# Kernel tuning notes

Measured on AMD Instinct MI355X. Metric: run time of the kernel, lower is better.

The kernel has to match this reference:

```python
import jax, jax.numpy as jnp
import numpy as np
from jax import lax

B, S, E = 512, 128, 7
H = 1024
PRED_LEN = 96


def setup_inputs() -> dict:
    key = jax.random.key(0)
    ks = jax.random.split(key, 10)
    u = lambda k, shape: jax.random.uniform(k, shape, jnp.float32, -0.1, 0.1)
    return {
        "x": jax.random.normal(ks[0], (B, S, E), jnp.float32),
        "Wi0": u(ks[1], (4 * H, E)),
        "Wh0": u(ks[2], (4 * H, H)),
        "b0": u(ks[3], (4 * H,)),
        "Wi1": u(ks[4], (4 * H, H)),
        "Wh1": u(ks[5], (4 * H, H)),
        "b1": u(ks[6], (4 * H,)),
        "Wfc": u(ks[7], (PRED_LEN * E, H)),
        "bfc": u(ks[8], (PRED_LEN * E,)),
    }


def _lstm_layer(xs, Wi, Wh, b):
    # xs: [B, S, in] -> hs: [B, S, H]; gate order i, f, g, o
    batch = xs.shape[0]
    hidden = Wh.shape[1]
    # precompute input projections for all timesteps in one big GEMM
    x_proj = jnp.einsum("bsi,gi->bsg", xs, Wi) + b  # [B, S, 4H]

    def step(carry, xp_t):
        h, c = carry
        gates = xp_t + h @ Wh.T  # [B, 4H]
        i_t, f_t, g_t, o_t = jnp.split(gates, 4, axis=-1)
        i_t = jax.nn.sigmoid(i_t)
        f_t = jax.nn.sigmoid(f_t)
        g_t = jnp.tanh(g_t)
        o_t = jax.nn.sigmoid(o_t)
        c = f_t * c + i_t * g_t
        h = o_t * jnp.tanh(c)
        return (h, c), h

    h0 = jnp.zeros((batch, hidden), xs.dtype)
    c0 = jnp.zeros((batch, hidden), xs.dtype)
    (_, _), hs = lax.scan(step, (h0, c0), jnp.swapaxes(x_proj, 0, 1))
    return jnp.swapaxes(hs, 0, 1)  # [B, S, H]


def reference(x, Wi0, Wh0, b0, Wi1, Wh1, b1, Wfc, bfc):
    h1 = _lstm_layer(x, Wi0, Wh0, b0)
    h2 = _lstm_layer(h1, Wi1, Wh1, b1)
    last = h2[:, -1, :]  # [B, H]
    pred = last @ Wfc.T + bfc  # [B, PRED_LEN*E]
    return pred.reshape(x.shape[0], PRED_LEN, E)
```

## Files before the change

### kernel.cpp

```cpp
#include <hip/hip_runtime.h>
#include <hip/hip_bf16.h>


typedef __bf16 bf16x8 __attribute__((ext_vector_type(8)));
typedef float  f32x4  __attribute__((ext_vector_type(4)));

#define HSZ   (512 * 1024)

__device__ __forceinline__ float sigm_f(float x) {
    x = fminf(30.f, fmaxf(-30.f, x));
    return 1.0f / (1.0f + __expf(-x));
}
__device__ __forceinline__ float tanh_f(float x) {
    x = fminf(30.f, fmaxf(-30.f, x));
    float e = __expf(-2.0f * x);
    return (1.0f - e) / (1.0f + e);
}

__device__ __forceinline__ int perm_row(int np) {
    int g = (np >> 4) & 3;
    int j = ((np >> 6) << 4) | (np & 15);
    return g * 1024 + j;
}

__device__ __forceinline__ void spin_ge(const int* p, int target) {
    while (__hip_atomic_load(p, __ATOMIC_RELAXED, __HIP_MEMORY_SCOPE_AGENT) < target)
        __builtin_amdgcn_s_sleep(1);
}
__device__ __forceinline__ void signal_inc(int* p) {
    __hip_atomic_fetch_add(p, 1, __ATOMIC_RELAXED, __HIP_MEMORY_SCOPE_AGENT);
}
__device__ __forceinline__ void inv_l1() {
    asm volatile("buffer_inv" ::: "memory");
}
__device__ __forceinline__ void store_ea(unsigned* p, unsigned v) {
    __hip_atomic_store(p, v, __ATOMIC_RELAXED, __HIP_MEMORY_SCOPE_AGENT);
}


__global__ void prep_w0(const float* __restrict__ Wh0, __bf16* __restrict__ W0p) {
    int idx = blockIdx.x * 256 + threadIdx.x;
    int np = idx >> 8, k4 = (idx & 255) << 2;
    int r = perm_row(np);
    float4 v = *(const float4*)(Wh0 + r * 1024 + k4);
    __bf16* o = W0p + np * 1024 + k4;
    o[0] = (__bf16)v.x; o[1] = (__bf16)v.y; o[2] = (__bf16)v.z; o[3] = (__bf16)v.w;
}

__global__ void prep_w1(const float* __restrict__ Wi1, const float* __restrict__ Wh1,
                        __bf16* __restrict__ W1p) {
    int idx = blockIdx.x * 256 + threadIdx.x;
    int np = idx >> 9, k4 = (idx & 511) << 2;
    int r = perm_row(np);
    const float* s = (k4 < 1024) ? (Wi1 + r * 1024 + k4) : (Wh1 + r * 1024 + (k4 - 1024));
    float4 v = *(const float4*)s;
    __bf16* o = W1p + np * 2048 + k4;
    o[0] = (__bf16)v.x; o[1] = (__bf16)v.y; o[2] = (__bf16)v.z; o[3] = (__bf16)v.w;
}

__global__ void prep_wfc(const float* __restrict__ Wfc, __bf16* __restrict__ Wfcp) {
    int idx = blockIdx.x * 256 + threadIdx.x;
    int n = idx >> 8, k4 = (idx & 255) << 2;
    __bf16* o = Wfcp + n * 1024 + k4;
    if (n < 672) {
        float4 v = *(const float4*)(Wfc + n * 1024 + k4);
        o[0] = (__bf16)v.x; o[1] = (__bf16)v.y; o[2] = (__bf16)v.z; o[3] = (__bf16)v.w;
    } else {
        o[0] = (__bf16)0.f; o[1] = (__bf16)0.f; o[2] = (__bf16)0.f; o[3] = (__bf16)0.f;
    }
}

__global__ void prep_small(const float* __restrict__ Wi0, const float* __restrict__ b0,
                           const float* __restrict__ b1,
                           float* __restrict__ Wi0p, float* __restrict__ b1p) {
    int np = blockIdx.x * 256 + threadIdx.x;
    int r = perm_row(np);
    float* o = Wi0p + np * 8;
    #pragma unroll
    for (int q = 0; q < 7; ++q) o[q] = Wi0[r * 7 + q];
    o[7] = b0[r];
    b1p[np] = b1[r];
}


template <bool D0, bool D1>
__device__ __forceinline__ void floop(const __bf16* __restrict__ abase,
                                      const __bf16* __restrict__ w0row,
                                      const __bf16* __restrict__ w1row,
                                      int tid,
                                      char* AldsB, char* B0ldsB, char* B1ldsB,
                                      f32x4 (&acc0)[4], f32x4 (&acc1)[4]) {
    const int a_r = tid >> 3;
    const int a_c = (tid & 7) << 3;
    const int b_r = tid >> 2;
    const int b_c = (tid & 3) << 4;
    const int l  = tid & 63, w = tid >> 6;
    const int wm = w & 3,   wn = w >> 2;
    const int lj = l & 15,  lq = l >> 4;
    const int r7 = lj & 7;

    const __bf16* arw = abase + a_r * 1024 + a_c;

    const int awr  = a_r * 128 + (((tid & 7) ^ (a_r & 7)) << 4);
    const int bwr0 = b_r * 128 + (((((tid & 3) << 1) | 0) ^ (b_r & 7)) << 4);
    const int bwr1 = b_r * 128 + (((((tid & 3) << 1) | 1) ^ (b_r & 7)) << 4);
    const int rc0 = ((lq     ) ^ r7) << 4;
    const int rc1 = ((lq | 4 ) ^ r7) << 4;

    uint4 ra, rb00, rb01, rb10, rb11;
    auto ld = [&](int k0) {
        ra = *(const uint4*)(arw + k0);
        if (D0) {
            const __bf16* p = w0row + k0;
            rb00 = *(const uint4*)(p);
            rb01 = *(const uint4*)(p + 8);
        }
        if (D1) {
            const __bf16* p = w1row + k0;
            rb10 = *(const uint4*)(p);
            rb11 = *(const uint4*)(p + 8);
        }
    };
    auto wr = [&](int buf) {
        *(uint4*)(AldsB + buf * 8192 + awr) = ra;
        if (D0) {
            char* Bl = B0ldsB + buf * 16384;
            *(uint4*)(Bl + bwr0) = rb00;
            *(uint4*)(Bl + bwr1) = rb01;
        }
        if (D1) {
            char* Bl = B1ldsB + buf * 16384;
            *(uint4*)(Bl + bwr0) = rb10;
            *(uint4*)(Bl + bwr1) = rb11;
        }
    };

    ld(0);
    wr(0);
    ld(64);
    __syncthreads();

    const char* Ap  = AldsB  + (wm * 16 + lj) * 128;
    const char* B0p = B0ldsB + (wn * 64 + lj) * 128;
    const char* B1p = B1ldsB + (wn * 64 + lj) * 128;

    for (int it = 0; it < 16; ++it) {
        const int bo = it & 1;
        const char* Ab  = Ap  + bo * 8192;
        const char* B0b = B0p + bo * 16384;
        const char* B1b = B1p + bo * 16384;
        #pragma unroll
        for (int s = 0; s < 2; ++s) {
            const int rc = s ? rc1 : rc0;
            bf16x8 af = *(const bf16x8*)(Ab + rc);
            #pragma unroll
            for (int ni = 0; ni < 4; ++ni) {
                if (D0) {
                    bf16x8 b0 = *(const bf16x8*)(B0b + ni * 2048 + rc);
                    acc0[ni] = __builtin_amdgcn_mfma_f32_16x16x32_bf16(af, b0, acc0[ni], 0, 0, 0);
                }
                if (D1) {
                    bf16x8 b1 = *(const bf16x8*)(B1b + ni * 2048 + rc);
                    acc1[ni] = __builtin_amdgcn_mfma_f32_16x16x32_bf16(af, b1, acc1[ni], 0, 0, 0);
                }
            }
        }
        if (it + 1 < 16) wr((it + 1) & 1);
        if (it + 2 < 16) ld((it + 2) * 64);
        __syncthreads();
    }
}


__global__ __launch_bounds__(512)
void lstm_persist(const float* __restrict__ x,
                  const __bf16* __restrict__ W0p, const __bf16* __restrict__ W1p,
                  const __bf16* __restrict__ Wfcp,
                  const float* __restrict__ Wi0p, const float* __restrict__ b1p,
                  const float* __restrict__ bfc,
                  __bf16* __restrict__ bufA, __bf16* __restrict__ bufB,
                  char* __restrict__ flagpage, float* __restrict__ out) {
    __shared__ __attribute__((aligned(16))) char Alds[2 * 8192];
    __shared__ __attribute__((aligned(16))) char B0lds[2 * 16384];
    __shared__ __attribute__((aligned(16))) char B1lds[2 * 16384];
    __shared__ float Aux1[128];
    __shared__ float Xlds[64 * 9];
    __shared__ float Wxlds[128 * 9];
    __shared__ int role[2];

    const int tid = threadIdx.x;

    if (tid == 0) {
        int xcd = __builtin_amdgcn_s_getreg(63508) & 7;
        int* xcnt = (int*)(flagpage + 1024) + xcd;
        int slot = __hip_atomic_fetch_add(xcnt, 1, __ATOMIC_RELAXED,
                                          __HIP_MEMORY_SCOPE_AGENT);
        role[0] = xcd; role[1] = slot;
    }
    __syncthreads();
    const int xcd = role[0];
    const int sl  = role[1];
    const int mt = sl >> 2, nb = sl & 3;
    const int m0 = mt * 64;
    const int n0 = xcd * 512 + nb * 128;
    int* cntA = (int*)(flagpage + (size_t)mt * 64);
    int* cntB = (int*)(flagpage + 512 + (size_t)mt * 64);

    if (tid < 128) {
        Aux1[tid] = b1p[n0 + tid];
    } else if (tid < 256) {
        int nl = tid - 128;
        const float* sp = Wi0p + (n0 + nl) * 8;
        float* d = Wxlds + nl * 9;
        #pragma unroll
        for (int q = 0; q < 8; ++q) d[q] = sp[q];
    }

    const int b_r = tid >> 2;
    const int b_c = (tid & 3) << 4;
    const int l  = tid & 63, w = tid >> 6;
    const int wm = w & 3,   wn = w >> 2;
    const int lj = l & 15,  lq = l >> 4;
    const int jc = (n0 >> 2) + wn * 16 + lj;

    const __bf16* w0row = W0p + (size_t)(n0 + b_r) * 1024 + b_c;
    const __bf16* w1row = W1p + (size_t)(n0 + b_r) * 2048 + b_c;

    float c0[4], c1[4];
    #pragma unroll
    for (int r = 0; r < 4; ++r) { c0[r] = 0.f; c1[r] = 0.f; }

    f32x4 acc0[4], acc1[4];

    for (int r = 0; r <= 128; ++r) {
        const bool do0 = (r < 128), do1 = (r > 0);
        const __bf16* haPrev = bufA + (size_t)(r % 3) * HSZ;
        __bf16*       haOut  = bufA + (size_t)((r + 1) % 3) * HSZ;
        const __bf16* hbPrev = bufB + (size_t)((r + 2) % 3) * HSZ;
        __bf16*       hbOut  = bufB + (size_t)(r % 3) * HSZ;

        if (tid == 0) spin_ge(cntA, 32 * r);
        __syncthreads();
        inv_l1();

        if (do0 && tid < 64) {
            const float* xr = x + (m0 + tid) * 896 + r * 7;
            float* d = Xlds + tid * 9;
            #pragma unroll
            for (int q = 0; q < 7; ++q) d[q] = xr[q];
            d[7] = 1.0f;
        }

        #pragma unroll
        for (int j = 0; j < 4; ++j) {
            acc0[j] = (f32x4){0.f, 0.f, 0.f, 0.f};
            acc1[j] = (f32x4){0.f, 0.f, 0.f, 0.f};
        }

        const __bf16* abase = haPrev + m0 * 1024;
        if (do0 && do1)
            floop<true, true >(abase, w0row, w1row, tid, Alds, B0lds, B1lds, acc0, acc1);
        else if (do0)
            floop<true, false>(abase, w0row, w1row, tid, Alds, B0lds, B1lds, acc0, acc1);
        else
            floop<false, true>(abase, w0row, w1row, tid, Alds, B0lds, B1lds, acc0, acc1);

        if (do0) {
            #pragma unroll
            for (int rr = 0; rr < 4; ++rr) {
                int ml = wm * 16 + lq * 4 + rr;
                int m  = m0 + ml;
                float pre[4];
                #pragma unroll
                for (int g = 0; g < 4; ++g) pre[g] = acc0[g][rr];
                const float* xr = Xlds + ml * 9;
                #pragma unroll
                for (int g = 0; g < 4; ++g) {
                    const float* wx = Wxlds + (wn * 64 + g * 16 + lj) * 9;
                    float sv = 0.f;
                    #pragma unroll
                    for (int q = 0; q < 8; ++q) sv += xr[q] * wx[q];
                    pre[g] += sv;
                }
                float ig = sigm_f(pre[0]);
                float fg = sigm_f(pre[1]);
                float gv = tanh_f(pre[2]);
                float og = sigm_f(pre[3]);
                float cn = fg * c0[rr] + ig * gv;
                c0[rr] = cn;
                float hv = og * tanh_f(cn);
                unsigned u32 = __builtin_bit_cast(unsigned, hv);
                unsigned hu = (u32 + 0x7fffu + ((u32 >> 16) & 1u)) >> 16;
                int pv = __shfl_xor((int)hu, 1, 64);
                if ((lj & 1) == 0)
                    store_ea((unsigned*)(haOut + (size_t)m * 1024 + jc),
                             hu | ((unsigned)pv << 16));
            }
        }
        __syncthreads();
        if (tid == 0) signal_inc(cntA);

        if (tid == 0) spin_ge(cntB, 32 * r);
        __syncthreads();
        inv_l1();

        if (do1) {
            floop<false, true>(hbPrev + m0 * 1024, w0row, w1row + 1024,
                               tid, Alds, B0lds, B1lds, acc0, acc1);

            #pragma unroll
            for (int rr = 0; rr < 4; ++rr) {
                int m = m0 + wm * 16 + lq * 4 + rr;
                float pre[4];
                #pragma unroll
                for (int g = 0; g < 4; ++g)
                    pre[g] = acc1[g][rr] + Aux1[wn * 64 + g * 16 + lj];
                float ig = sigm_f(pre[0]);
                float fg = sigm_f(pre[1]);
                float gv = tanh_f(pre[2]);
                float og = sigm_f(pre[3]);
                float cn = fg * c1[rr] + ig * gv;
                c1[rr] = cn;
                float hv = og * tanh_f(cn);
                unsigned u32 = __builtin_bit_cast(unsigned, hv);
                unsigned hu = (u32 + 0x7fffu + ((u32 >> 16) & 1u)) >> 16;
                int pv = __shfl_xor((int)hu, 1, 64);
                if ((lj & 1) == 0)
                    store_ea((unsigned*)(hbOut + (size_t)m * 1024 + jc),
                             hu | ((unsigned)pv << 16));
            }
        }
        __syncthreads();
        if (tid == 0) signal_inc(cntB);
    }

    if (nb == 0 && xcd < 6) {
        const int n0fc = xcd * 128;
        if (tid == 0) spin_ge(cntB, 32 * 129);
        __syncthreads();
        inv_l1();
        if (tid < 128) {
            int n = n0fc + tid;
            Aux1[tid] = (n < 672) ? bfc[n] : 0.f;
        }
        #pragma unroll
        for (int j = 0; j < 4; ++j)
            acc0[j] = (f32x4){0.f, 0.f, 0.f, 0.f};
        floop<true, false>(bufB + (size_t)2 * HSZ + m0 * 1024,
                           Wfcp + (size_t)(n0fc + b_r) * 1024 + b_c, nullptr,
                           tid, Alds, B0lds, B1lds, acc0, acc1);
        #pragma unroll
        for (int rr = 0; rr < 4; ++rr) {
            int m = m0 + wm * 16 + lq * 4 + rr;
            #pragma unroll
            for (int ni = 0; ni < 4; ++ni) {
                int n = n0fc + wn * 64 + ni * 16 + lj;
                if (n < 672)
                    out[m * 672 + n] = acc0[ni][rr] + Aux1[wn * 64 + ni * 16 + lj];
            }
        }
    }
}

#define O_W0P   0u
#define O_W1P   8388608u
#define O_WFCP  25165824u
#define O_WI0P  26738688u
#define O_B1P   26869760u
#define O_FLG   26886144u
#define O_BA    26888192u
#define O_BB    30033920u
#define WS_NEED 33179648u

extern "C" void kernel_launch(void* const* d_in, const int* in_sizes, int n_in,
                              void* d_out, int out_size, void* d_ws, size_t ws_size,
                              hipStream_t stream) {
    const float* x   = (const float*)d_in[0];
    const float* Wi0 = (const float*)d_in[1];
    const float* Wh0 = (const float*)d_in[2];
    const float* b0  = (const float*)d_in[3];
    const float* Wi1 = (const float*)d_in[4];
    const float* Wh1 = (const float*)d_in[5];
    const float* b1  = (const float*)d_in[6];
    const float* Wfc = (const float*)d_in[7];
    const float* bfc = (const float*)d_in[8];
    float* out = (float*)d_out;
    char*  ws  = (char*)d_ws;
    if (ws_size < WS_NEED) return;

    __bf16* W0p  = (__bf16*)(ws + O_W0P);
    __bf16* W1p  = (__bf16*)(ws + O_W1P);
    __bf16* Wfcp = (__bf16*)(ws + O_WFCP);
    float*  Wi0p = (float*)(ws + O_WI0P);
    float*  b1p  = (float*)(ws + O_B1P);
    char*   flg  = (char*)(ws + O_FLG);
    __bf16* bufA = (__bf16*)(ws + O_BA);
    __bf16* bufB = (__bf16*)(ws + O_BB);

    hipMemsetAsync(ws + O_FLG, 0, 2048u + 1048576u, stream);
    hipMemsetAsync(ws + O_BB, 0, 1048576u, stream);

    prep_w0   <<<4096, 256, 0, stream>>>(Wh0, W0p);
    prep_w1   <<<8192, 256, 0, stream>>>(Wi1, Wh1, W1p);
    prep_wfc  <<<768,  256, 0, stream>>>(Wfc, Wfcp);
    prep_small<<<16,   256, 0, stream>>>(Wi0, b0, b1, Wi0p, b1p);

    lstm_persist<<<256, 512, 0, stream>>>(x, W0p, W1p, Wfcp, Wi0p, b1p, bfc,
                                          bufA, bufB, flg, out);
}
```

Measured before the change: 2.828 ms.

## Split the layer-1 recurrent GEMM across a second half-block with an LDS reduction

The persistent LSTM kernel now runs 1024 threads per block. The upper 512 threads compute layer 1's recurrent h_b·Wh1 product concurrently with the lower half's layer-0 and input-projection GEMMs, then add their partial sums into the lower half's accumulators through LDS. Both step counters are waited on once at the start of each step, which removes the second spin/sync phase per step and shortens the serial chain. The costs are a tighter register budget at 1024 threads (possible spills), extra LDS use, and matched dummy floop calls needed to keep the barrier counts consistent across the two halves.

New measurement: 2.999 ms. +6.1%, slower.

```diff
diff --git a/kernel.cpp b/kernel.cpp
--- a/kernel.cpp
+++ b/kernel.cpp
@@ -172,7 +172,7 @@
 }
 
 
-__global__ __launch_bounds__(512)
+__global__ __launch_bounds__(1024)
 void lstm_persist(const float* __restrict__ x,
                   const __bf16* __restrict__ W0p, const __bf16* __restrict__ W1p,
                   const __bf16* __restrict__ Wfcp,
@@ -183,12 +183,16 @@
     __shared__ __attribute__((aligned(16))) char Alds[2 * 8192];
     __shared__ __attribute__((aligned(16))) char B0lds[2 * 16384];
     __shared__ __attribute__((aligned(16))) char B1lds[2 * 16384];
+    __shared__ __attribute__((aligned(16))) char A2lds[2 * 8192];
+    __shared__ __attribute__((aligned(16))) char B1bls[2 * 16384];
     __shared__ float Aux1[128];
     __shared__ float Xlds[64 * 9];
     __shared__ float Wxlds[128 * 9];
     __shared__ int role[2];
 
-    const int tid = threadIdx.x;
+    const int tid  = threadIdx.x;
+    const int half = tid >> 9;
+    const int t5   = tid & 511;
 
     if (tid == 0) {
         int xcd = __builtin_amdgcn_s_getreg(63508) & 7;
@@ -216,9 +220,9 @@
         for (int q = 0; q < 8; ++q) d[q] = sp[q];
     }
 
-    const int b_r = tid >> 2;
-    const int b_c = (tid & 3) << 4;
-    const int l  = tid & 63, w = tid >> 6;
+    const int b_r = t5 >> 2;
+    const int b_c = (t5 & 3) << 4;
+    const int l  = t5 & 63, w = t5 >> 6;
     const int wm = w & 3,   wn = w >> 2;
     const int lj = l & 15,  lq = l >> 4;
     const int jc = (n0 >> 2) + wn * 16 + lj;
@@ -239,7 +243,7 @@
         const __bf16* hbPrev = bufB + (size_t)((r + 2) % 3) * HSZ;
         __bf16*       hbOut  = bufB + (size_t)(r % 3) * HSZ;
 
-        if (tid == 0) spin_ge(cntA, 32 * r);
+        if (tid == 0) { spin_ge(cntA, 32 * r); spin_ge(cntB, 32 * r); }
         __syncthreads();
         inv_l1();
 
@@ -257,15 +261,29 @@
             acc1[j] = (f32x4){0.f, 0.f, 0.f, 0.f};
         }
 
-        const __bf16* abase = haPrev + m0 * 1024;
-        if (do0 && do1)
-            floop<true, true >(abase, w0row, w1row, tid, Alds, B0lds, B1lds, acc0, acc1);
-        else if (do0)
-            floop<true, false>(abase, w0row, w1row, tid, Alds, B0lds, B1lds, acc0, acc1);
-        else
-            floop<false, true>(abase, w0row, w1row, tid, Alds, B0lds, B1lds, acc0, acc1);
-
-        if (do0) {
+        if (half == 0) {
+            const __bf16* abase = haPrev + m0 * 1024;
+            if (do0 && do1)
+                floop<true, true >(abase, w0row, w1row, t5, Alds, B0lds, B1lds, acc0, acc1);
+            else if (do0)
+                floop<true, false>(abase, w0row, w1row, t5, Alds, B0lds, B1lds, acc0, acc1);
+            else
+                floop<false, true>(abase, w0row, w1row, t5, Alds, B0lds, B1lds, acc0, acc1);
+        } else {
+            const __bf16* abase2 = hbPrev + m0 * 1024;
+            if (do1)
+                floop<false, true >(abase2, w0row, w1row + 1024, t5, A2lds, B0lds, B1bls, acc0, acc1);
+            else
+                floop<false, false>(abase2, w0row, w1row, t5, A2lds, B0lds, B1bls, acc0, acc1);
+        }
+
+        if (half == 1 && do1) {
+            #pragma unroll
+            for (int j = 0; j < 4; ++j)
+                *(f32x4*)(B0lds + t5 * 64 + j * 16) = acc1[j];
+        }
+
+        if (half == 0 && do0) {
             #pragma unroll
             for (int rr = 0; rr < 4; ++rr) {
                 int ml = wm * 16 + lq * 4 + rr;
@@ -300,14 +318,13 @@
         __syncthreads();
         if (tid == 0) signal_inc(cntA);
 
-        if (tid == 0) spin_ge(cntB, 32 * r);
-        __syncthreads();
-        inv_l1();
-
-        if (do1) {
-            floop<false, true>(hbPrev + m0 * 1024, w0row, w1row + 1024,
-                               tid, Alds, B0lds, B1lds, acc0, acc1);
-
+        if (half == 0 && do1) {
+            #pragma unroll
+            for (int j = 0; j < 4; ++j) {
+                f32x4 p = *(const f32x4*)(B0lds + t5 * 64 + j * 16);
+                acc1[j][0] += p[0]; acc1[j][1] += p[1];
+                acc1[j][2] += p[2]; acc1[j][3] += p[3];
+            }
             #pragma unroll
             for (int rr = 0; rr < 4; ++rr) {
                 int m = m0 + wm * 16 + lq * 4 + rr;
@@ -346,17 +363,23 @@
         #pragma unroll
         for (int j = 0; j < 4; ++j)
             acc0[j] = (f32x4){0.f, 0.f, 0.f, 0.f};
-        floop<true, false>(bufB + (size_t)2 * HSZ + m0 * 1024,
-                           Wfcp + (size_t)(n0fc + b_r) * 1024 + b_c, nullptr,
-                           tid, Alds, B0lds, B1lds, acc0, acc1);
-        #pragma unroll
-        for (int rr = 0; rr < 4; ++rr) {
-            int m = m0 + wm * 16 + lq * 4 + rr;
-            #pragma unroll
-            for (int ni = 0; ni < 4; ++ni) {
-                int n = n0fc + wn * 64 + ni * 16 + lj;
-                if (n < 672)
-                    out[m * 672 + n] = acc0[ni][rr] + Aux1[wn * 64 + ni * 16 + lj];
+        if (half == 0)
+            floop<true, false>(bufB + (size_t)2 * HSZ + m0 * 1024,
+                               Wfcp + (size_t)(n0fc + b_r) * 1024 + b_c, nullptr,
+                               t5, Alds, B0lds, B1lds, acc0, acc1);
+        else
+            floop<false, false>(bufB + (size_t)2 * HSZ + m0 * 1024,
+                                w0row, w1row, t5, A2lds, B0lds, B1bls, acc0, acc1);
+        if (half == 0) {
+            #pragma unroll
+            for (int rr = 0; rr < 4; ++rr) {
+                int m = m0 + wm * 16 + lq * 4 + rr;
+                #pragma unroll
+                for (int ni = 0; ni < 4; ++ni) {
+                    int n = n0fc + wn * 64 + ni * 16 + lj;
+                    if (n < 672)
+                        out[m * 672 + n] = acc0[ni][rr] + Aux1[wn * 64 + ni * 16 + lj];
+                }
             }
         }
     }
@@ -405,6 +428,6 @@
     prep_wfc  <<<768,  256, 0, stream>>>(Wfc, Wfcp);
     prep_small<<<16,   256, 0, stream>>>(Wi0, b0, b1, Wi0p, b1p);
 
-    lstm_persist<<<256, 512, 0, stream>>>(x, W0p, W1p, Wfcp, Wi0p, b1p, bfc,
-                                          bufA, bufB, flg, out);
-}
+    lstm_persist<<<256, 1024, 0, stream>>>(x, W0p, W1p, Wfcp, Wi0p, b1p, bfc,
+                                           bufA, bufB, flg, out);
+}
```

## Fuse layer-1 recurrent GEMM into the main K-loop and drop one grid barrier

Applied to the files above, without the earlier changes.

The layer-1 recurrent GEMM (h2_prev · Wh1) now runs inside the same K-loop as the layer-0 recurrence and the layer-1 input projection. It uses extra LDS buffers for the second A operand and its weights. This removes one grid-wide spin wait and one full K-loop pass per timestep, at the cost of more LDS, more registers and more load traffic per iteration. Both counters are now waited on up front, which could lengthen the critical path and lower occupancy.

New measurement: 2.959 ms. 4.6% more time.

```diff
diff --git a/kernel.cpp b/kernel.cpp
--- a/kernel.cpp
+++ b/kernel.cpp
@@ -83,13 +83,16 @@
 }
 
 
-template <bool D0, bool D1>
-__device__ __forceinline__ void floop(const __bf16* __restrict__ abase,
-                                      const __bf16* __restrict__ w0row,
-                                      const __bf16* __restrict__ w1row,
-                                      int tid,
-                                      char* AldsB, char* B0ldsB, char* B1ldsB,
-                                      f32x4 (&acc0)[4], f32x4 (&acc1)[4]) {
+template <bool D0, bool D1, bool D2>
+__device__ __forceinline__ void floopf(const __bf16* __restrict__ abase,
+                                       const __bf16* __restrict__ abase2,
+                                       const __bf16* __restrict__ w0row,
+                                       const __bf16* __restrict__ w1row,
+                                       const __bf16* __restrict__ w1rowB,
+                                       int tid,
+                                       char* AldsB, char* B0ldsB, char* B1ldsB,
+                                       char* A2ldsB, char* B1bldsB,
+                                       f32x4 (&acc0)[4], f32x4 (&acc1)[4]) {
     const int a_r = tid >> 3;
     const int a_c = (tid & 7) << 3;
     const int b_r = tid >> 2;
@@ -99,7 +102,8 @@
     const int lj = l & 15,  lq = l >> 4;
     const int r7 = lj & 7;
 
-    const __bf16* arw = abase + a_r * 1024 + a_c;
+    const __bf16* arw  = abase  + a_r * 1024 + a_c;
+    const __bf16* arw2 = abase2 + a_r * 1024 + a_c;
 
     const int awr  = a_r * 128 + (((tid & 7) ^ (a_r & 7)) << 4);
     const int bwr0 = b_r * 128 + (((((tid & 3) << 1) | 0) ^ (b_r & 7)) << 4);
@@ -108,6 +112,7 @@
     const int rc1 = ((lq | 4 ) ^ r7) << 4;
 
     uint4 ra, rb00, rb01, rb10, rb11;
+    uint4 ra2, rc10, rc11;
     auto ld = [&](int k0) {
         ra = *(const uint4*)(arw + k0);
         if (D0) {
@@ -119,6 +124,12 @@
             const __bf16* p = w1row + k0;
             rb10 = *(const uint4*)(p);
             rb11 = *(const uint4*)(p + 8);
+        }
+        if (D2) {
+            ra2 = *(const uint4*)(arw2 + k0);
+            const __bf16* p = w1rowB + k0;
+            rc10 = *(const uint4*)(p);
+            rc11 = *(const uint4*)(p + 8);
         }
     };
     auto wr = [&](int buf) {
@@ -133,6 +144,12 @@
             *(uint4*)(Bl + bwr0) = rb10;
             *(uint4*)(Bl + bwr1) = rb11;
         }
+        if (D2) {
+            *(uint4*)(A2ldsB + buf * 8192 + awr) = ra2;
+            char* Bl = B1bldsB + buf * 16384;
+            *(uint4*)(Bl + bwr0) = rc10;
+            *(uint4*)(Bl + bwr1) = rc11;
+        }
     };
 
     ld(0);
@@ -140,19 +157,25 @@
     ld(64);
     __syncthreads();
 
-    const char* Ap  = AldsB  + (wm * 16 + lj) * 128;
-    const char* B0p = B0ldsB + (wn * 64 + lj) * 128;
-    const char* B1p = B1ldsB + (wn * 64 + lj) * 128;
+    const char* Ap   = AldsB   + (wm * 16 + lj) * 128;
+    const char* A2p  = A2ldsB  + (wm * 16 + lj) * 128;
+    const char* B0p  = B0ldsB  + (wn * 64 + lj) * 128;
+    const char* B1p  = B1ldsB  + (wn * 64 + lj) * 128;
+    const char* B1bp = B1bldsB + (wn * 64 + lj) * 128;
 
     for (int it = 0; it < 16; ++it) {
         const int bo = it & 1;
-        const char* Ab  = Ap  + bo * 8192;
-        const char* B0b = B0p + bo * 16384;
-        const char* B1b = B1p + bo * 16384;
+        const char* Ab   = Ap   + bo * 8192;
+        const char* A2b  = A2p  + bo * 8192;
+        const char* B0b  = B0p  + bo * 16384;
+        const char* B1b  = B1p  + bo * 16384;
+        const char* B1bb = B1bp + bo * 16384;
         #pragma unroll
         for (int s = 0; s < 2; ++s) {
             const int rc = s ? rc1 : rc0;
             bf16x8 af = *(const bf16x8*)(Ab + rc);
+            bf16x8 af2;
+            if (D2) af2 = *(const bf16x8*)(A2b + rc);
             #pragma unroll
             for (int ni = 0; ni < 4; ++ni) {
                 if (D0) {
@@ -162,6 +185,10 @@
                 if (D1) {
                     bf16x8 b1 = *(const bf16x8*)(B1b + ni * 2048 + rc);
                     acc1[ni] = __builtin_amdgcn_mfma_f32_16x16x32_bf16(af, b1, acc1[ni], 0, 0, 0);
+                }
+                if (D2) {
+                    bf16x8 b2 = *(const bf16x8*)(B1bb + ni * 2048 + rc);
+                    acc1[ni] = __builtin_amdgcn_mfma_f32_16x16x32_bf16(af2, b2, acc1[ni], 0, 0, 0);
                 }
             }
         }
@@ -183,6 +210,8 @@
     __shared__ __attribute__((aligned(16))) char Alds[2 * 8192];
     __shared__ __attribute__((aligned(16))) char B0lds[2 * 16384];
     __shared__ __attribute__((aligned(16))) char B1lds[2 * 16384];
+    __shared__ __attribute__((aligned(16))) char A2lds[2 * 8192];
+    __shared__ __attribute__((aligned(16))) char B1blds[2 * 16384];
     __shared__ float Aux1[128];
     __shared__ float Xlds[64 * 9];
     __shared__ float Wxlds[128 * 9];
@@ -239,7 +268,7 @@
         const __bf16* hbPrev = bufB + (size_t)((r + 2) % 3) * HSZ;
         __bf16*       hbOut  = bufB + (size_t)(r % 3) * HSZ;
 
-        if (tid == 0) spin_ge(cntA, 32 * r);
+        if (tid == 0) { spin_ge(cntA, 32 * r); spin_ge(cntB, 32 * r); }
         __syncthreads();
         inv_l1();
 
@@ -257,13 +286,17 @@
             acc1[j] = (f32x4){0.f, 0.f, 0.f, 0.f};
         }
 
-        const __bf16* abase = haPrev + m0 * 1024;
+        const __bf16* abase  = haPrev + m0 * 1024;
+        const __bf16* abase2 = hbPrev + m0 * 1024;
         if (do0 && do1)
-            floop<true, true >(abase, w0row, w1row, tid, Alds, B0lds, B1lds, acc0, acc1);
+            floopf<true, true, true >(abase, abase2, w0row, w1row, w1row + 1024,
+                                      tid, Alds, B0lds, B1lds, A2lds, B1blds, acc0, acc1);
         else if (do0)
-            floop<true, false>(abase, w0row, w1row, tid, Alds, B0lds, B1lds, acc0, acc1);
+            floopf<true, false, false>(abase, abase2, w0row, w1row, w1row + 1024,
+                                       tid, Alds, B0lds, B1lds, A2lds, B1blds, acc0, acc1);
         else
-            floop<false, true>(abase, w0row, w1row, tid, Alds, B0lds, B1lds, acc0, acc1);
+            floopf<false, true, true>(abase, abase2, w0row, w1row, w1row + 1024,
+                                      tid, Alds, B0lds, B1lds, A2lds, B1blds, acc0, acc1);
 
         if (do0) {
             #pragma unroll
@@ -300,14 +333,7 @@
         __syncthreads();
         if (tid == 0) signal_inc(cntA);
 
-        if (tid == 0) spin_ge(cntB, 32 * r);
-        __syncthreads();
-        inv_l1();
-
         if (do1) {
-            floop<false, true>(hbPrev + m0 * 1024, w0row, w1row + 1024,
-                               tid, Alds, B0lds, B1lds, acc0, acc1);
-
             #pragma unroll
             for (int rr = 0; rr < 4; ++rr) {
                 int m = m0 + wm * 16 + lq * 4 + rr;
@@ -346,9 +372,11 @@
         #pragma unroll
         for (int j = 0; j < 4; ++j)
             acc0[j] = (f32x4){0.f, 0.f, 0.f, 0.f};
-        floop<true, false>(bufB + (size_t)2 * HSZ + m0 * 1024,
-                           Wfcp + (size_t)(n0fc + b_r) * 1024 + b_c, nullptr,
-                           tid, Alds, B0lds, B1lds, acc0, acc1);
+        const __bf16* hfin = bufB + (size_t)2 * HSZ + m0 * 1024;
+        floopf<true, false, false>(hfin, hfin,
+                                   Wfcp + (size_t)(n0fc + b_r) * 1024 + b_c,
+                                   w1row, w1row + 1024,
+                                   tid, Alds, B0lds, B1lds, A2lds, B1blds, acc0, acc1);
         #pragma unroll
         for (int rr = 0; rr < 4; ++rr) {
             int m = m0 + wm * 16 + lq * 4 + rr;
```
